# Performance work log

Measured on AMD Instinct MI355X. Metric: run time of the kernel, lower is better.

## Reference

```python
import jax, jax.numpy as jnp
import numpy as np

B, T, C = 2, 2048, 2048
H = 16
ROPE_DIM, NOPE_DIM, V_DIM = 64, 64, 128
HEAD_DIM = NOPE_DIM + ROPE_DIM  # 128
Q_RANK, KV_RANK = 1536, 512


def setup_inputs() -> dict:
    key = jax.random.key(0)
    ks = jax.random.split(key, 8)
    std = 0.02
    return {
        "x": jax.random.normal(ks[0], (B, T, C), jnp.float32),
        "cos": jax.random.normal(ks[1], (1, T, 1, ROPE_DIM // 2), jnp.float32),
        "sin": jax.random.normal(ks[2], (1, T, 1, ROPE_DIM // 2), jnp.float32),
        "wq_down": jax.random.normal(ks[3], (Q_RANK, C), jnp.float32) * std,
        "wq_up": jax.random.normal(ks[4], (H * HEAD_DIM, Q_RANK), jnp.float32) * std,
        "wkv_down": jax.random.normal(ks[5], (KV_RANK, C), jnp.float32) * std,
        "wkv_up": jax.random.normal(ks[6], (H * (HEAD_DIM + V_DIM), KV_RANK), jnp.float32) * std,
        "wo": jax.random.normal(ks[7], (C, H * V_DIM), jnp.float32) * std,
    }


def _rope(x, cos, sin):
    # x: [B, T, H, rope_dim]
    d = x.shape[-1] // 2
    x1, x2 = x[..., :d], x[..., d:]
    return jnp.concatenate([x1 * cos + x2 * sin, -x1 * sin + x2 * cos], axis=-1)


def _rms_norm(x):
    eps = jnp.finfo(x.dtype).eps
    return x * jax.lax.rsqrt(jnp.mean(jnp.square(x), axis=-1, keepdims=True) + eps)


def reference(x, cos, sin, wq_down, wq_up, wkv_down, wkv_up, wo):
    # Low-rank q projection
    q = jnp.einsum('btc,rc,dr->btd', x, wq_down, wq_up)
    q = q.reshape(B, T, H, HEAD_DIM)
    q_nope, q_rope = q[..., :NOPE_DIM], q[..., NOPE_DIM:]
    # Low-rank kv projection (naive decompression)
    kv = jnp.einsum('btc,rc,dr->btd', x, wkv_down, wkv_up)
    kv = kv.reshape(B, T, H, HEAD_DIM + V_DIM)
    k_nope = kv[..., :NOPE_DIM]
    k_rope = kv[..., NOPE_DIM:HEAD_DIM]
    v = kv[..., HEAD_DIM:]
    # Partial RoPE on the rope sub-dims only
    q_rope = _rope(q_rope, cos, sin)
    k_rope = _rope(k_rope, cos, sin)
    q = _rms_norm(jnp.concatenate([q_nope, q_rope], axis=-1))
    k = _rms_norm(jnp.concatenate([k_nope, k_rope], axis=-1))
    # Causal SDPA: [B, H, T, T]
    scale = 1.0 / jnp.sqrt(jnp.float32(HEAD_DIM))
    scores = jnp.einsum('bthd,bshd->bhts', q, k) * scale
    causal = jnp.tril(jnp.ones((T, T), dtype=bool))
    scores = jnp.where(causal, scores, jnp.finfo(scores.dtype).min)
    probs = jax.nn.softmax(scores, axis=-1)
    y = jnp.einsum('bhts,bshd->bthd', probs, v).reshape(B, T, H * V_DIM)
    return y @ wo.T
```

## Files before the change

### kernel.cpp

```cpp
#include <hip/hip_runtime.h>
#include <hip/hip_bf16.h>
#include <math.h>
#include <type_traits>

#define AS1 __attribute__((address_space(1)))
#define AS3 __attribute__((address_space(3)))

typedef __bf16  bf16x8 __attribute__((ext_vector_type(8)));
typedef float   f32x4  __attribute__((ext_vector_type(4)));
typedef __hip_bfloat16 bf16;

#define MFMA16x16x32 __builtin_amdgcn_mfma_f32_16x16x32_bf16

__device__ __forceinline__ void gload16(const void* g, void* l) {
  __builtin_amdgcn_global_load_lds((const AS1 void*)g, (AS3 void*)l, 16, 0, 0);
}

__global__ __launch_bounds__(256) void f2bf_kernel(const float4* __restrict__ in,
                                                   ushort4* __restrict__ out, int n4) {
  int i = blockIdx.x * 256 + threadIdx.x;
  if (i >= n4) return;
  float4 v = in[i];
  ushort4 o;
  o.x = __builtin_bit_cast(unsigned short, __float2bfloat16(v.x));
  o.y = __builtin_bit_cast(unsigned short, __float2bfloat16(v.y));
  o.z = __builtin_bit_cast(unsigned short, __float2bfloat16(v.z));
  o.w = __builtin_bit_cast(unsigned short, __float2bfloat16(v.w));
  out[i] = o;
}

template <typename OutT>
__global__ __launch_bounds__(256, 3) void gemm_bt(const bf16* __restrict__ A,
                                                  const bf16* __restrict__ W,
                                                  OutT* __restrict__ Cp,
                                                  int M, int N, int K) {
  __shared__ __align__(16) bf16 As[128 * 32];
  __shared__ __align__(16) bf16 Ws[128 * 32];
  const int t = threadIdx.x;
  const int w = t >> 6, lane = t & 63;
  const int quad = lane >> 4, l16 = lane & 15;
  const int wr = (w >> 1) * 64, wc = (w & 1) * 64;
  const size_t m0 = (size_t)blockIdx.x * 128;
  const size_t n0 = (size_t)blockIdx.y * 128;

  const int rowS = t >> 2;
  const int kch  = (t & 3) * 8;

  f32x4 acc[4][4];
#pragma unroll
  for (int i = 0; i < 4; i++)
#pragma unroll
    for (int j = 0; j < 4; j++) acc[i][j] = f32x4{0.f, 0.f, 0.f, 0.f};

  for (int k0 = 0; k0 < K; k0 += 32) {
    __syncthreads();
    gload16(A + (m0 + rowS) * K + k0 + kch,        (char*)As + w * 1024);
    gload16(A + (m0 + rowS + 64) * K + k0 + kch,   (char*)As + 4096 + w * 1024);
    gload16(W + (n0 + rowS) * K + k0 + kch,        (char*)Ws + w * 1024);
    gload16(W + (n0 + rowS + 64) * K + k0 + kch,   (char*)Ws + 4096 + w * 1024);
    __syncthreads();

    bf16x8 af[4], bw[4];
#pragma unroll
    for (int i = 0; i < 4; i++)
      af[i] = *(const bf16x8*)(As + (wr + i * 16 + l16) * 32 + quad * 8);
#pragma unroll
    for (int j = 0; j < 4; j++)
      bw[j] = *(const bf16x8*)(Ws + (wc + j * 16 + l16) * 32 + quad * 8);
#pragma unroll
    for (int i = 0; i < 4; i++)
#pragma unroll
      for (int j = 0; j < 4; j++)
        acc[i][j] = MFMA16x16x32(af[i], bw[j], acc[i][j], 0, 0, 0);
  }

#pragma unroll
  for (int i = 0; i < 4; i++)
#pragma unroll
    for (int j = 0; j < 4; j++)
#pragma unroll
      for (int r = 0; r < 4; r++) {
        size_t row = m0 + wr + i * 16 + quad * 4 + r;
        size_t col = n0 + wc + j * 16 + l16;
        float v = acc[i][j][r];
        if constexpr (std::is_same<OutT, float>::value)
          Cp[row * N + col] = v;
        else
          Cp[row * N + col] = __float2bfloat16(v);
      }
}

__global__ __launch_bounds__(256) void rope_rms(const bf16* __restrict__ qraw,
                                                const bf16* __restrict__ kvraw,
                                                const float* __restrict__ cosp,
                                                const float* __restrict__ sinp,
                                                bf16* __restrict__ qn,
                                                bf16* __restrict__ kn) {
  const int bt = blockIdx.x;
  const int w = threadIdx.x >> 6, lane = threadIdx.x & 63;
  const int h = blockIdx.y * 4 + w;
  const int tt = bt & 2047;
  const float c = cosp[tt * 32 + (lane & 31)];
  const float s = sinp[tt * 32 + (lane & 31)];
  const float inv128 = 1.0f / 128.0f;
  const float eps = 1.1920929e-7f;

  {
    const bf16* base = qraw + (size_t)bt * 2048 + h * 128;
    float a = (float)base[lane];
    float o = (float)base[64 + lane];
    float partner = __shfl_xor(o, 32);
    float orope = (lane < 32) ? (o * c + partner * s) : (o * c - partner * s);
    float ss = a * a + orope * orope;
#pragma unroll
    for (int off = 1; off < 64; off <<= 1) ss += __shfl_xor(ss, off);
    float rn = rsqrtf(ss * inv128 + eps);
    bf16* outp = qn + ((size_t)bt * 16 + h) * 128;
    outp[lane] = __float2bfloat16(a * rn);
    outp[64 + lane] = __float2bfloat16(orope * rn);
  }
  {
    const bf16* base = kvraw + (size_t)bt * 4096 + h * 256;
    float a = (float)base[lane];
    float o = (float)base[64 + lane];
    float partner = __shfl_xor(o, 32);
    float orope = (lane < 32) ? (o * c + partner * s) : (o * c - partner * s);
    float ss = a * a + orope * orope;
#pragma unroll
    for (int off = 1; off < 64; off <<= 1) ss += __shfl_xor(ss, off);
    float rn = rsqrtf(ss * inv128 + eps);
    bf16* outp = kn + ((size_t)bt * 16 + h) * 128;
    outp[lane] = __float2bfloat16(a * rn);
    outp[64 + lane] = __float2bfloat16(orope * rn);
  }
}

__global__ __launch_bounds__(256) void vtrans(const bf16* __restrict__ kvraw,
                                              bf16* __restrict__ vT) {
  __shared__ __align__(16) bf16 tile[64][72];
  const int b = blockIdx.z >> 4, h = blockIdx.z & 15;
  const int t0 = blockIdx.x * 64, d0 = blockIdx.y * 64;
  const int tr = threadIdx.x >> 2;
  const int cc = (threadIdx.x & 3) << 4;

  const bf16* src = kvraw + ((size_t)(b * 2048 + t0 + tr)) * 4096 + h * 256 + 128 + d0 + cc;
  *(uint4*)&tile[tr][cc]     = *(const uint4*)(src);
  *(uint4*)&tile[tr][cc + 8] = *(const uint4*)(src + 8);
  __syncthreads();

  __align__(16) bf16 tmp[16];
#pragma unroll
  for (int j = 0; j < 16; j++) tmp[j] = tile[cc + j][tr];
  bf16* dst = vT + ((size_t)blockIdx.z * 128 + d0 + tr) * 2048 + t0 + cc;
  *(uint4*)dst       = *(const uint4*)&tmp[0];
  *(uint4*)(dst + 8) = *(const uint4*)&tmp[8];
}

__global__ __launch_bounds__(256, 3) void attn_kernel(const bf16* __restrict__ qn,
                                                      const bf16* __restrict__ kn,
                                                      const bf16* __restrict__ vT,
                                                      bf16* __restrict__ y) {
  __shared__ __align__(16) bf16 Ks[64 * 128];
  __shared__ __align__(16) bf16 Vs[128 * 64];
  __shared__ __align__(16) bf16 Ps[4 * 16 * 72];
  const int t = threadIdx.x, w = t >> 6, lane = t & 63;
  const int quad = lane >> 4, l16 = lane & 15;
  const int b = blockIdx.x >> 4, h = blockIdx.x & 15;
  const int xb = 31 - (int)blockIdx.y;
  const int q0 = xb * 64;
  const int T_ = 2048, H_ = 16;

  bf16x8 qf[4];
  {
    const bf16* qbase = qn + ((size_t)(b * T_ + q0 + w * 16 + l16) * H_ + h) * 128;
#pragma unroll
    for (int ks = 0; ks < 4; ks++) qf[ks] = *(const bf16x8*)(qbase + ks * 32 + quad * 8);
  }
  f32x4 yacc[8];
#pragma unroll
  for (int i = 0; i < 8; i++) yacc[i] = f32x4{0.f, 0.f, 0.f, 0.f};
  float lrow[4] = {0.f, 0.f, 0.f, 0.f};
  const float K1 = 0.08838834764831845f * 1.4426950408889634f;
  const float K2 = -12.0f * 1.4426950408889634f;
  const int ntiles = xb + 1;

  for (int it = 0; it < ntiles; ++it) {
    const int s0 = it * 64;
    __syncthreads();
#pragma unroll
    for (int is = 0; is < 4; ++is) {
      int srow = is * 16 + w * 4 + quad;
      int cg = l16 ^ (srow & 7);
      gload16(kn + ((size_t)(b * T_ + s0 + srow) * H_ + h) * 128 + cg * 8,
              (char*)Ks + is * 4096 + w * 1024);
    }
#pragma unroll
    for (int is = 0; is < 4; ++is) {
      int drow = is * 32 + w * 8 + (lane >> 3);
      int cg = (lane & 7) ^ (drow & 7);
      gload16(vT + ((size_t)(b * H_ + h) * 128 + drow) * T_ + s0 + cg * 8,
              (char*)Vs + is * 4096 + w * 1024);
    }
    __syncthreads();

    f32x4 sacc[4];
#pragma unroll
    for (int cg = 0; cg < 4; cg++) sacc[cg] = f32x4{0.f, 0.f, 0.f, 0.f};
#pragma unroll
    for (int cg = 0; cg < 4; ++cg) {
      const int srow = cg * 16 + l16;
#pragma unroll
      for (int ks = 0; ks < 4; ++ks) {
        int pos = (ks * 4 + quad) ^ (srow & 7);
        bf16x8 kf = *(const bf16x8*)(Ks + srow * 128 + pos * 8);
        sacc[cg] = MFMA16x16x32(qf[ks], kf, sacc[cg], 0, 0, 0);
      }
    }

    const bool diag = (it == ntiles - 1);
    float p[4][4];
#pragma unroll
    for (int cg = 0; cg < 4; ++cg)
#pragma unroll
      for (int r = 0; r < 4; ++r) {
        float e;
        if (diag && (cg * 16 + l16 > w * 16 + quad * 4 + r))
          e = 0.0f;
        else
          e = exp2f(fmaf(sacc[cg][r], K1, K2));
        p[cg][r] = e;
        lrow[r] += e;
      }

#pragma unroll
    for (int cg = 0; cg < 4; cg++)
#pragma unroll
      for (int r = 0; r < 4; r++)
        Ps[w * 1152 + (quad * 4 + r) * 72 + cg * 16 + l16] = __float2bfloat16(p[cg][r]);
    __asm__ volatile("s_waitcnt lgkmcnt(0)" ::: "memory");

    bf16x8 pf[2];
#pragma unroll
    for (int k2 = 0; k2 < 2; k2++)
      pf[k2] = *(const bf16x8*)(Ps + w * 1152 + l16 * 72 + k2 * 32 + quad * 8);
#pragma unroll
    for (int dg = 0; dg < 8; dg++) {
      const int drow = dg * 16 + l16;
#pragma unroll
      for (int k2 = 0; k2 < 2; k2++) {
        int pos = (k2 * 4 + quad) ^ (drow & 7);
        bf16x8 vf = *(const bf16x8*)(Vs + drow * 64 + pos * 8);
        yacc[dg] = MFMA16x16x32(pf[k2], vf, yacc[dg], 0, 0, 0);
      }
    }
  }

#pragma unroll
  for (int off = 1; off < 16; off <<= 1)
#pragma unroll
    for (int r = 0; r < 4; r++) lrow[r] += __shfl_xor(lrow[r], off);
#pragma unroll
  for (int r = 0; r < 4; r++) {
    float inv = 1.0f / lrow[r];
    size_t qrow = (size_t)(b * T_ + q0 + w * 16 + quad * 4 + r);
    bf16* outp = y + qrow * 2048 + h * 128;
#pragma unroll
    for (int dg = 0; dg < 8; dg++)
      outp[dg * 16 + l16] = __float2bfloat16(yacc[dg][r] * inv);
  }
}

extern "C" void kernel_launch(void* const* d_in, const int* in_sizes, int n_in,
                              void* d_out, int out_size, void* d_ws, size_t ws_size,
                              hipStream_t stream) {
  (void)in_sizes; (void)n_in; (void)out_size; (void)ws_size;
  const float* x    = (const float*)d_in[0];
  const float* cosp = (const float*)d_in[1];
  const float* sinp = (const float*)d_in[2];
  const float* wqd  = (const float*)d_in[3];
  const float* wqu  = (const float*)d_in[4];
  const float* wkvd = (const float*)d_in[5];
  const float* wkvu = (const float*)d_in[6];
  const float* wo   = (const float*)d_in[7];
  float* out = (float*)d_out;

  char* ws = (char*)d_ws;
  size_t off = 0;
  auto alloc = [&](size_t elems) { bf16* p = (bf16*)(ws + off); off += elems * 2; return p; };
  bf16* xb     = alloc((size_t)4096 * 2048);
  bf16* wqdB   = alloc((size_t)1536 * 2048);
  bf16* wquB   = alloc((size_t)2048 * 1536);
  bf16* wkvdB  = alloc((size_t)512 * 2048);
  bf16* wkvuB  = alloc((size_t)4096 * 512);
  bf16* woB    = alloc((size_t)2048 * 2048);
  bf16* qdown  = alloc((size_t)4096 * 1536);
  bf16* kvdown = alloc((size_t)4096 * 512);
  bf16* qraw   = alloc((size_t)4096 * 2048);
  bf16* kvraw  = alloc((size_t)4096 * 4096);
  bf16* qnb    = alloc((size_t)4096 * 16 * 128);
  bf16* knb    = alloc((size_t)4096 * 16 * 128);
  bf16* vTb    = alloc((size_t)2 * 16 * 128 * 2048);
  bf16* yb     = alloc((size_t)4096 * 2048);

  auto conv = [&](const float* src, bf16* dst, size_t n) {
    f2bf_kernel<<<dim3((unsigned)(n / 1024)), dim3(256), 0, stream>>>(
        (const float4*)src, (ushort4*)dst, (int)(n / 4));
  };
  conv(x,    xb,    (size_t)4096 * 2048);
  conv(wqd,  wqdB,  (size_t)1536 * 2048);
  conv(wqu,  wquB,  (size_t)2048 * 1536);
  conv(wkvd, wkvdB, (size_t)512 * 2048);
  conv(wkvu, wkvuB, (size_t)4096 * 512);
  conv(wo,   woB,   (size_t)2048 * 2048);

  gemm_bt<bf16><<<dim3(32, 12), 256, 0, stream>>>(xb, wqdB, qdown, 4096, 1536, 2048);
  gemm_bt<bf16><<<dim3(32, 4),  256, 0, stream>>>(xb, wkvdB, kvdown, 4096, 512, 2048);
  gemm_bt<bf16><<<dim3(32, 16), 256, 0, stream>>>(qdown, wquB, qraw, 4096, 2048, 1536);
  gemm_bt<bf16><<<dim3(32, 32), 256, 0, stream>>>(kvdown, wkvuB, kvraw, 4096, 4096, 512);
  rope_rms<<<dim3(4096, 4), 256, 0, stream>>>(qraw, kvraw, cosp, sinp, qnb, knb);
  vtrans<<<dim3(32, 2, 32), 256, 0, stream>>>(kvraw, vTb);
  attn_kernel<<<dim3(32, 32), 256, 0, stream>>>(qnb, knb, vTb, yb);
  gemm_bt<float><<<dim3(32, 16), 256, 0, stream>>>(yb, woB, out, 4096, 2048, 2048);
}
```

Before: 416.9 us.

## Use 32x32 MFMA with 128-row query tiles, merge casts and down-projections

The six fp32-to-bf16 casts become one multi-buffer cast launch. The q and kv down-projection GEMMs merge into one GEMM by placing the two weights contiguously, with a lda parameter for the strided up-projection inputs. The attention kernel is restructured so each block handles 128 query rows, using 32x32x16 MFMAs and a swizzled P buffer. Block ordering is changed to balance the causal work, and occupancy is lowered to 2. The aim is fewer launches, less redundant K/V loading per query, and denser MFMA issue, at the cost of more registers per thread.

```diff
diff --git a/kernel.cpp b/kernel.cpp
--- a/kernel.cpp
+++ b/kernel.cpp
@@ -8,32 +8,46 @@
 
 typedef __bf16  bf16x8 __attribute__((ext_vector_type(8)));
 typedef float   f32x4  __attribute__((ext_vector_type(4)));
+typedef float   f32x16 __attribute__((ext_vector_type(16)));
 typedef __hip_bfloat16 bf16;
 
 #define MFMA16x16x32 __builtin_amdgcn_mfma_f32_16x16x32_bf16
+#define MFMA32x32x16 __builtin_amdgcn_mfma_f32_32x32x16_bf16
 
 __device__ __forceinline__ void gload16(const void* g, void* l) {
   __builtin_amdgcn_global_load_lds((const AS1 void*)g, (AS3 void*)l, 16, 0, 0);
 }
 
-__global__ __launch_bounds__(256) void f2bf_kernel(const float4* __restrict__ in,
-                                                   ushort4* __restrict__ out, int n4) {
-  int i = blockIdx.x * 256 + threadIdx.x;
-  if (i >= n4) return;
-  float4 v = in[i];
+struct CastArgs {
+  const float4* src[6];
+  ushort4* dst[6];
+  unsigned bound[6];
+};
+
+__global__ __launch_bounds__(256) void f2bf_multi(CastArgs a) {
+  unsigned i = blockIdx.x * 256 + threadIdx.x;
+  if (i >= a.bound[5]) return;
+  unsigned lo = 0;
+  int s = 0;
+#pragma unroll
+  for (int k = 0; k < 5; k++) {
+    if (i >= a.bound[k]) { s = k + 1; lo = a.bound[k]; }
+  }
+  unsigned idx = i - lo;
+  float4 v = a.src[s][idx];
   ushort4 o;
   o.x = __builtin_bit_cast(unsigned short, __float2bfloat16(v.x));
   o.y = __builtin_bit_cast(unsigned short, __float2bfloat16(v.y));
   o.z = __builtin_bit_cast(unsigned short, __float2bfloat16(v.z));
   o.w = __builtin_bit_cast(unsigned short, __float2bfloat16(v.w));
-  out[i] = o;
+  a.dst[s][idx] = o;
 }
 
 template <typename OutT>
 __global__ __launch_bounds__(256, 3) void gemm_bt(const bf16* __restrict__ A,
                                                   const bf16* __restrict__ W,
                                                   OutT* __restrict__ Cp,
-                                                  int M, int N, int K) {
+                                                  int M, int N, int K, int lda) {
   __shared__ __align__(16) bf16 As[128 * 32];
   __shared__ __align__(16) bf16 Ws[128 * 32];
   const int t = threadIdx.x;
@@ -54,10 +68,10 @@
 
   for (int k0 = 0; k0 < K; k0 += 32) {
     __syncthreads();
-    gload16(A + (m0 + rowS) * K + k0 + kch,        (char*)As + w * 1024);
-    gload16(A + (m0 + rowS + 64) * K + k0 + kch,   (char*)As + 4096 + w * 1024);
-    gload16(W + (n0 + rowS) * K + k0 + kch,        (char*)Ws + w * 1024);
-    gload16(W + (n0 + rowS + 64) * K + k0 + kch,   (char*)Ws + 4096 + w * 1024);
+    gload16(A + (m0 + rowS) * (size_t)lda + k0 + kch,      (char*)As + w * 1024);
+    gload16(A + (m0 + rowS + 64) * (size_t)lda + k0 + kch, (char*)As + 4096 + w * 1024);
+    gload16(W + (n0 + rowS) * (size_t)K + k0 + kch,        (char*)Ws + w * 1024);
+    gload16(W + (n0 + rowS + 64) * (size_t)K + k0 + kch,   (char*)Ws + 4096 + w * 1024);
     __syncthreads();
 
     bf16x8 af[4], bw[4];
@@ -156,41 +170,48 @@
   *(uint4*)(dst + 8) = *(const uint4*)&tmp[8];
 }
 
-__global__ __launch_bounds__(256, 3) void attn_kernel(const bf16* __restrict__ qn,
+__global__ __launch_bounds__(256, 2) void attn_kernel(const bf16* __restrict__ qn,
                                                       const bf16* __restrict__ kn,
                                                       const bf16* __restrict__ vT,
                                                       bf16* __restrict__ y) {
   __shared__ __align__(16) bf16 Ks[64 * 128];
   __shared__ __align__(16) bf16 Vs[128 * 64];
-  __shared__ __align__(16) bf16 Ps[4 * 16 * 72];
+  __shared__ __align__(16) bf16 Ps[4][32 * 64];
   const int t = threadIdx.x, w = t >> 6, lane = t & 63;
-  const int quad = lane >> 4, l16 = lane & 15;
+  const int l32 = lane & 31, hl = lane >> 5;
   const int b = blockIdx.x >> 4, h = blockIdx.x & 15;
-  const int xb = 31 - (int)blockIdx.y;
-  const int q0 = xb * 64;
+  const int yy = blockIdx.y;
+  const int xb = (yy < 8) ? (15 - yy) : (yy - 8);
+  const int q0 = xb * 128;
   const int T_ = 2048, H_ = 16;
 
-  bf16x8 qf[4];
+  bf16x8 qf[8];
   {
-    const bf16* qbase = qn + ((size_t)(b * T_ + q0 + w * 16 + l16) * H_ + h) * 128;
-#pragma unroll
-    for (int ks = 0; ks < 4; ks++) qf[ks] = *(const bf16x8*)(qbase + ks * 32 + quad * 8);
-  }
-  f32x4 yacc[8];
-#pragma unroll
-  for (int i = 0; i < 8; i++) yacc[i] = f32x4{0.f, 0.f, 0.f, 0.f};
-  float lrow[4] = {0.f, 0.f, 0.f, 0.f};
+    const bf16* qbase = qn + ((size_t)(b * T_ + q0 + w * 32 + l32) * H_ + h) * 128;
+#pragma unroll
+    for (int ki = 0; ki < 8; ki++)
+      qf[ki] = *(const bf16x8*)(qbase + (ki * 2 + hl) * 8);
+  }
+
+  f32x16 yacc[4];
+#pragma unroll
+  for (int db = 0; db < 4; db++)
+#pragma unroll
+    for (int i = 0; i < 16; i++) yacc[db][i] = 0.f;
+  float lrow[16];
+#pragma unroll
+  for (int r = 0; r < 16; r++) lrow[r] = 0.f;
   const float K1 = 0.08838834764831845f * 1.4426950408889634f;
   const float K2 = -12.0f * 1.4426950408889634f;
-  const int ntiles = xb + 1;
+  const int ntiles = 2 * xb + 2;
 
   for (int it = 0; it < ntiles; ++it) {
     const int s0 = it * 64;
     __syncthreads();
 #pragma unroll
     for (int is = 0; is < 4; ++is) {
-      int srow = is * 16 + w * 4 + quad;
-      int cg = l16 ^ (srow & 7);
+      int srow = is * 16 + w * 4 + (lane >> 4);
+      int cg = (lane & 15) ^ (srow & 7);
       gload16(kn + ((size_t)(b * T_ + s0 + srow) * H_ + h) * 128 + cg * 8,
               (char*)Ks + is * 4096 + w * 1024);
     }
@@ -203,70 +224,70 @@
     }
     __syncthreads();
 
-    f32x4 sacc[4];
-#pragma unroll
-    for (int cg = 0; cg < 4; cg++) sacc[cg] = f32x4{0.f, 0.f, 0.f, 0.f};
-#pragma unroll
-    for (int cg = 0; cg < 4; ++cg) {
-      const int srow = cg * 16 + l16;
-#pragma unroll
-      for (int ks = 0; ks < 4; ++ks) {
-        int pos = (ks * 4 + quad) ^ (srow & 7);
-        bf16x8 kf = *(const bf16x8*)(Ks + srow * 128 + pos * 8);
-        sacc[cg] = MFMA16x16x32(qf[ks], kf, sacc[cg], 0, 0, 0);
+    f32x16 sacc[2];
+#pragma unroll
+    for (int cb = 0; cb < 2; cb++)
+#pragma unroll
+      for (int i = 0; i < 16; i++) sacc[cb][i] = 0.f;
+#pragma unroll
+    for (int cb = 0; cb < 2; ++cb) {
+      const int s = cb * 32 + l32;
+#pragma unroll
+      for (int ki = 0; ki < 8; ++ki) {
+        int pos = (ki * 2 + hl) ^ (s & 7);
+        bf16x8 kf = *(const bf16x8*)(Ks + s * 128 + pos * 8);
+        sacc[cb] = MFMA32x32x16(qf[ki], kf, sacc[cb], 0, 0, 0);
       }
     }
 
-    const bool diag = (it == ntiles - 1);
-    float p[4][4];
-#pragma unroll
-    for (int cg = 0; cg < 4; ++cg)
-#pragma unroll
-      for (int r = 0; r < 4; ++r) {
+    const bool diag = (it >= ntiles - 2);
+#pragma unroll
+    for (int cb = 0; cb < 2; ++cb) {
+      const int sidx = cb * 32 + l32;
+      const int sg = s0 + sidx;
+#pragma unroll
+      for (int r = 0; r < 16; ++r) {
+        const int row = (r & 3) + 8 * (r >> 2) + 4 * hl;
         float e;
-        if (diag && (cg * 16 + l16 > w * 16 + quad * 4 + r))
+        if (diag && (sg > q0 + w * 32 + row))
           e = 0.0f;
         else
-          e = exp2f(fmaf(sacc[cg][r], K1, K2));
-        p[cg][r] = e;
+          e = exp2f(fmaf(sacc[cb][r], K1, K2));
         lrow[r] += e;
+        Ps[w][row * 64 + (((sidx >> 3) ^ (row & 7)) << 3) + (sidx & 7)] =
+            __float2bfloat16(e);
       }
-
-#pragma unroll
-    for (int cg = 0; cg < 4; cg++)
-#pragma unroll
-      for (int r = 0; r < 4; r++)
-        Ps[w * 1152 + (quad * 4 + r) * 72 + cg * 16 + l16] = __float2bfloat16(p[cg][r]);
+    }
     __asm__ volatile("s_waitcnt lgkmcnt(0)" ::: "memory");
 
-    bf16x8 pf[2];
-#pragma unroll
-    for (int k2 = 0; k2 < 2; k2++)
-      pf[k2] = *(const bf16x8*)(Ps + w * 1152 + l16 * 72 + k2 * 32 + quad * 8);
-#pragma unroll
-    for (int dg = 0; dg < 8; dg++) {
-      const int drow = dg * 16 + l16;
-#pragma unroll
-      for (int k2 = 0; k2 < 2; k2++) {
-        int pos = (k2 * 4 + quad) ^ (drow & 7);
-        bf16x8 vf = *(const bf16x8*)(Vs + drow * 64 + pos * 8);
-        yacc[dg] = MFMA16x16x32(pf[k2], vf, yacc[dg], 0, 0, 0);
+#pragma unroll
+    for (int ki = 0; ki < 4; ++ki) {
+      int ppos = (ki * 2 + hl) ^ (l32 & 7);
+      bf16x8 pf = *(const bf16x8*)(&Ps[w][l32 * 64 + ppos * 8]);
+#pragma unroll
+      for (int db = 0; db < 4; ++db) {
+        int d = db * 32 + l32;
+        int vpos = (ki * 2 + hl) ^ (d & 7);
+        bf16x8 vf = *(const bf16x8*)(Vs + d * 64 + vpos * 8);
+        yacc[db] = MFMA32x32x16(pf, vf, yacc[db], 0, 0, 0);
       }
     }
   }
 
 #pragma unroll
-  for (int off = 1; off < 16; off <<= 1)
-#pragma unroll
-    for (int r = 0; r < 4; r++) lrow[r] += __shfl_xor(lrow[r], off);
-#pragma unroll
-  for (int r = 0; r < 4; r++) {
+  for (int r = 0; r < 16; r++) {
+#pragma unroll
+    for (int off = 1; off < 32; off <<= 1) lrow[r] += __shfl_xor(lrow[r], off);
+  }
+#pragma unroll
+  for (int r = 0; r < 16; r++) {
+    const int row = (r & 3) + 8 * (r >> 2) + 4 * hl;
     float inv = 1.0f / lrow[r];
-    size_t qrow = (size_t)(b * T_ + q0 + w * 16 + quad * 4 + r);
+    size_t qrow = (size_t)(b * T_ + q0 + w * 32 + row);
     bf16* outp = y + qrow * 2048 + h * 128;
 #pragma unroll
-    for (int dg = 0; dg < 8; dg++)
-      outp[dg * 16 + l16] = __float2bfloat16(yacc[dg][r] * inv);
+    for (int db = 0; db < 4; db++)
+      outp[db * 32 + l32] = __float2bfloat16(yacc[db][r] * inv);
   }
 }
 
@@ -287,38 +308,39 @@
   char* ws = (char*)d_ws;
   size_t off = 0;
   auto alloc = [&](size_t elems) { bf16* p = (bf16*)(ws + off); off += elems * 2; return p; };
-  bf16* xb     = alloc((size_t)4096 * 2048);
-  bf16* wqdB   = alloc((size_t)1536 * 2048);
-  bf16* wquB   = alloc((size_t)2048 * 1536);
-  bf16* wkvdB  = alloc((size_t)512 * 2048);
-  bf16* wkvuB  = alloc((size_t)4096 * 512);
-  bf16* woB    = alloc((size_t)2048 * 2048);
-  bf16* qdown  = alloc((size_t)4096 * 1536);
-  bf16* kvdown = alloc((size_t)4096 * 512);
-  bf16* qraw   = alloc((size_t)4096 * 2048);
-  bf16* kvraw  = alloc((size_t)4096 * 4096);
-  bf16* qnb    = alloc((size_t)4096 * 16 * 128);
-  bf16* knb    = alloc((size_t)4096 * 16 * 128);
-  bf16* vTb    = alloc((size_t)2 * 16 * 128 * 2048);
-  bf16* yb     = alloc((size_t)4096 * 2048);
-
-  auto conv = [&](const float* src, bf16* dst, size_t n) {
-    f2bf_kernel<<<dim3((unsigned)(n / 1024)), dim3(256), 0, stream>>>(
-        (const float4*)src, (ushort4*)dst, (int)(n / 4));
-  };
-  conv(x,    xb,    (size_t)4096 * 2048);
-  conv(wqd,  wqdB,  (size_t)1536 * 2048);
-  conv(wqu,  wquB,  (size_t)2048 * 1536);
-  conv(wkvd, wkvdB, (size_t)512 * 2048);
-  conv(wkvu, wkvuB, (size_t)4096 * 512);
-  conv(wo,   woB,   (size_t)2048 * 2048);
-
-  gemm_bt<bf16><<<dim3(32, 12), 256, 0, stream>>>(xb, wqdB, qdown, 4096, 1536, 2048);
-  gemm_bt<bf16><<<dim3(32, 4),  256, 0, stream>>>(xb, wkvdB, kvdown, 4096, 512, 2048);
-  gemm_bt<bf16><<<dim3(32, 16), 256, 0, stream>>>(qdown, wquB, qraw, 4096, 2048, 1536);
-  gemm_bt<bf16><<<dim3(32, 32), 256, 0, stream>>>(kvdown, wkvuB, kvraw, 4096, 4096, 512);
+  bf16* xb      = alloc((size_t)4096 * 2048);
+  bf16* wqdB    = alloc((size_t)1536 * 2048);
+  bf16* wkvdB   = alloc((size_t)512 * 2048);
+  bf16* wquB    = alloc((size_t)2048 * 1536);
+  bf16* wkvuB   = alloc((size_t)4096 * 512);
+  bf16* woB     = alloc((size_t)2048 * 2048);
+  bf16* qkvdown = alloc((size_t)4096 * 2048);
+  bf16* qraw    = alloc((size_t)4096 * 2048);
+  bf16* kvraw   = alloc((size_t)4096 * 4096);
+  bf16* qnb     = alloc((size_t)4096 * 16 * 128);
+  bf16* knb     = alloc((size_t)4096 * 16 * 128);
+  bf16* vTb     = alloc((size_t)2 * 16 * 128 * 2048);
+  bf16* yb      = alloc((size_t)4096 * 2048);
+
+  CastArgs ca;
+  const float* srcs[6] = {x, wqd, wkvd, wqu, wkvu, wo};
+  bf16* dsts[6]        = {xb, wqdB, wkvdB, wquB, wkvuB, woB};
+  size_t cnts[6] = {(size_t)4096 * 2048, (size_t)1536 * 2048, (size_t)512 * 2048,
+                    (size_t)2048 * 1536, (size_t)4096 * 512,  (size_t)2048 * 2048};
+  unsigned cum = 0;
+  for (int i = 0; i < 6; i++) {
+    ca.src[i] = (const float4*)srcs[i];
+    ca.dst[i] = (ushort4*)dsts[i];
+    cum += (unsigned)(cnts[i] / 4);
+    ca.bound[i] = cum;
+  }
+  f2bf_multi<<<dim3((cum + 255) / 256), 256, 0, stream>>>(ca);
+
+  gemm_bt<bf16><<<dim3(32, 16), 256, 0, stream>>>(xb, wqdB, qkvdown, 4096, 2048, 2048, 2048);
+  gemm_bt<bf16><<<dim3(32, 16), 256, 0, stream>>>(qkvdown, wquB, qraw, 4096, 2048, 1536, 2048);
+  gemm_bt<bf16><<<dim3(32, 32), 256, 0, stream>>>(qkvdown + 1536, wkvuB, kvraw, 4096, 4096, 512, 2048);
   rope_rms<<<dim3(4096, 4), 256, 0, stream>>>(qraw, kvraw, cosp, sinp, qnb, knb);
   vtrans<<<dim3(32, 2, 32), 256, 0, stream>>>(kvraw, vTb);
-  attn_kernel<<<dim3(32, 32), 256, 0, stream>>>(qnb, knb, vTb, yb);
-  gemm_bt<float><<<dim3(32, 16), 256, 0, stream>>>(yb, woB, out, 4096, 2048, 2048);
-}
+  attn_kernel<<<dim3(32, 16), 256, 0, stream>>>(qnb, knb, vTb, yb);
+  gemm_bt<float><<<dim3(32, 16), 256, 0, stream>>>(yb, woB, out, 4096, 2048, 2048, 2048);
+}
```

Measured after the change: 391.5 us. -6.1%, faster.
